# Optimization experiments

Measured on AMD Instinct MI355X. Metric: run time of the kernel, lower is better.

Reference implementation:

```python
import jax, jax.numpy as jnp
import numpy as np

N_NODES = 50000
N_EDGES = 800000


def sage_conv(x, src, dst, W_l, b_l, W_r, num_nodes):
    """PyG SAGEConv with mean aggregation: out = lin_l(mean_agg(neighbors)) + lin_r(x)."""
    # gather source-node features per edge, scatter-mean into destination nodes
    msg = x[src]                                                   # [E, F]
    agg = jax.ops.segment_sum(msg, dst, num_segments=num_nodes)    # [N, F]
    cnt = jax.ops.segment_sum(jnp.ones((src.shape[0],), x.dtype), dst,
                              num_segments=num_nodes)              # [N]
    agg = agg / jnp.maximum(cnt, 1.0)[:, None]
    return agg @ W_l + b_l + x @ W_r


def setup_inputs() -> dict:
    key = jax.random.key(0)
    ks = jax.random.split(key, 8)
    d_in, d_hid, d_out = 128, 256, 128
    s = lambda k, shape, fan: jax.random.normal(k, shape, jnp.float32) / np.sqrt(fan)
    return {
        "x": jax.random.normal(ks[0], (N_NODES, d_in), jnp.float32),
        "edge_index": jax.random.randint(ks[1], (2, N_EDGES), 0, N_NODES, jnp.int64),
        "W1_l": s(ks[2], (d_in, d_hid), d_in),
        "b1": jnp.zeros((d_hid,), jnp.float32),
        "W1_r": s(ks[3], (d_in, d_hid), d_in),
        "W2_l": s(ks[4], (d_hid, d_out), d_hid),
        "b2": jnp.zeros((d_out,), jnp.float32),
        "W2_r": s(ks[5], (d_hid, d_out), d_hid),
    }


def reference(x, edge_index, W1_l, b1, W1_r, W2_l, b2, W2_r):
    src, dst = edge_index[0], edge_index[1]
    n = x.shape[0]
    h = sage_conv(x, src, dst, W1_l, b1, W1_r, n)
    h = jax.nn.relu(h)  # dropout p=0.0 -> identity
    out = sage_conv(h, src, dst, W2_l, b2, W2_r, n)
    return out
```

## Files before the change

kernel.cpp:

```cpp
#include <hip/hip_runtime.h>
#include <hip/hip_bf16.h>
#include <stdint.h>

#define NN 50000
#define NE 800000
#define NB 196
#define EPB 2048
#define NBLK ((NE + EPB - 1) / EPB)

typedef __attribute__((ext_vector_type(8))) __bf16 bf16x8;
typedef __attribute__((ext_vector_type(4))) float f32x4;

__device__ __forceinline__ float bflo(uint32_t u) { return __uint_as_float(u << 16); }
__device__ __forceinline__ float bfhi(uint32_t u) { return __uint_as_float(u & 0xffff0000u); }
__device__ __forceinline__ uint16_t f2bf(float f) {
    uint32_t u = __float_as_uint(f);
    u += 0x7fffu + ((u >> 16) & 1u);
    return (uint16_t)(u >> 16);
}
__device__ __forceinline__ float bf2f(uint16_t h) { return __uint_as_float(((uint32_t)h) << 16); }

__global__ __launch_bounds__(256) void detect(const uint32_t* __restrict__ xu,
                                              const int* __restrict__ ei,
                                              int* __restrict__ flags) {
    __shared__ int cnt_f, cnt_i;
    if (threadIdx.x == 0) { cnt_f = 0; cnt_i = 0; }
    __syncthreads();
    uint32_t u = xu[threadIdx.x];
    uint32_t lo = u & 0xffffu;
    uint32_t e = (lo >> 7) & 0xffu;
    int ok = (lo == 0u) || (e >= 96u && e <= 150u);
    atomicAdd(&cnt_f, ok);
    if (threadIdx.x < 64) {
        int w = ei[2 * threadIdx.x + 1];
        atomicAdd(&cnt_i, (w != 0) ? 1 : 0);
    }
    __syncthreads();
    if (threadIdx.x == 0) {
        flags[0] = (cnt_f < 192) ? 1 : 0;
        flags[1] = (cnt_i < 4) ? 1 : 0;
    }
}

__global__ __launch_bounds__(256) void hist_pass(const int* __restrict__ ei, const int* __restrict__ flags,
                                                 int* __restrict__ histM) {
    __shared__ int hist[NB];
    for (int i = threadIdx.x; i < NB; i += 256) hist[i] = 0;
    __syncthreads();
    int base = blockIdx.x * EPB;
    int fl = flags[1];
    for (int i = 0; i < EPB; i += 256) {
        int e = base + i + threadIdx.x;
        if (e < NE) {
            int d = fl ? ei[2 * NE + 2 * e] : ei[NE + e];
            atomicAdd(&hist[d >> 8], 1);
        }
    }
    __syncthreads();
    for (int i = threadIdx.x; i < NB; i += 256) histM[i * NBLK + blockIdx.x] = hist[i];
}

__global__ __launch_bounds__(512) void scan_rows(int* __restrict__ histM, int* __restrict__ bucket_tot) {
    __shared__ int sm[512];
    int b = blockIdx.x, t = threadIdx.x;
    int v = (t < NBLK) ? histM[b * NBLK + t] : 0;
    sm[t] = v;
    __syncthreads();
    for (int o = 1; o < 512; o <<= 1) {
        int x = (t >= o) ? sm[t - o] : 0;
        __syncthreads();
        sm[t] += x;
        __syncthreads();
    }
    if (t < NBLK) histM[b * NBLK + t] = sm[t] - v;
    if (t == 511) bucket_tot[b] = sm[511];
}

__global__ __launch_bounds__(256) void scan_tot(const int* __restrict__ bucket_tot, int* __restrict__ bucket_base) {
    __shared__ int sm[256];
    int t = threadIdx.x;
    int v = (t < NB) ? bucket_tot[t] : 0;
    sm[t] = v;
    __syncthreads();
    for (int o = 1; o < 256; o <<= 1) {
        int x = (t >= o) ? sm[t - o] : 0;
        __syncthreads();
        sm[t] += x;
        __syncthreads();
    }
    if (t < NB) bucket_base[t] = sm[t] - v;
    if (t == 0) bucket_base[NB] = NE;
}

__global__ __launch_bounds__(256) void scatter_pass(const int* __restrict__ ei, const int* __restrict__ flags,
                                                    const int* __restrict__ histM, const int* __restrict__ bucket_base,
                                                    uint32_t* __restrict__ staging) {
    __shared__ int curs[NB];
    int blk = blockIdx.x, t = threadIdx.x;
    for (int i = t; i < NB; i += 256) curs[i] = bucket_base[i] + histM[i * NBLK + blk];
    __syncthreads();
    int base = blk * EPB;
    int fl = flags[1];
    for (int i = 0; i < EPB; i += 256) {
        int e = base + i + t;
        if (e < NE) {
            int s, d;
            if (fl) { s = ei[2 * e]; d = ei[2 * NE + 2 * e]; }
            else    { s = ei[e];     d = ei[NE + e]; }
            int p = atomicAdd(&curs[d >> 8], 1);
            staging[p] = ((uint32_t)(d & 0xff) << 16) | (uint32_t)s;
        }
    }
}

__global__ __launch_bounds__(256) void build_csr(const uint32_t* __restrict__ staging,
                                                 const int* __restrict__ bucket_base,
                                                 int* __restrict__ row_start, int* __restrict__ deg,
                                                 float* __restrict__ inv_deg, int* __restrict__ csr) {
    __shared__ int degs[256];
    __shared__ int sm[256];
    __shared__ int curs[256];
    int b = blockIdx.x, t = threadIdx.x;
    int beg = bucket_base[b], cnt = bucket_base[b + 1] - beg;
    degs[t] = 0;
    __syncthreads();
    for (int i = t; i < cnt; i += 256) atomicAdd(&degs[(staging[beg + i] >> 16) & 0xff], 1);
    __syncthreads();
    int d = degs[t];
    sm[t] = d;
    __syncthreads();
    for (int o = 1; o < 256; o <<= 1) {
        int x = (t >= o) ? sm[t - o] : 0;
        __syncthreads();
        sm[t] += x;
        __syncthreads();
    }
    int excl = sm[t] - d;
    curs[t] = excl;
    int node = b * 256 + t;
    if (node < NN) {
        row_start[node] = beg + excl;
        deg[node] = d;
        inv_deg[node] = 1.0f / (float)(d > 0 ? d : 1);
    }
    __syncthreads();
    for (int i = t; i < cnt; i += 256) {
        uint32_t u = staging[beg + i];
        int dl = (u >> 16) & 0xff;
        int p = atomicAdd(&curs[dl], 1);
        csr[beg + p] = (int)(u & 0xffffu);
    }
}

__global__ __launch_bounds__(256) void norm_x(const void* __restrict__ x, const int* __restrict__ flags,
                                              uint32_t* __restrict__ out) {
    int i = blockIdx.x * 256 + threadIdx.x;
    if (flags[0]) {
        float2 v = ((const float2*)x)[i];
        out[i] = (uint32_t)f2bf(v.x) | ((uint32_t)f2bf(v.y) << 16);
    } else {
        out[i] = ((const uint32_t*)x)[i];
    }
}

__global__ __launch_bounds__(256) void norm_weights_sw(const void* __restrict__ w1l, const void* __restrict__ b1,
                                                       const void* __restrict__ w1r, const void* __restrict__ w2l,
                                                       const void* __restrict__ b2, const void* __restrict__ w2r,
                                                       const int* __restrict__ flags,
                                                       uint16_t* __restrict__ w1l_sw, uint16_t* __restrict__ w1r_sw,
                                                       uint16_t* __restrict__ w2l_sw, uint16_t* __restrict__ w2r_sw,
                                                       uint16_t* __restrict__ bias_buf) {
    int tid = blockIdx.x * 256 + threadIdx.x;
    int fp32 = flags[0];
    if (tid < 16384) {
        int frag = tid >> 6, lane = tid & 63;
        const void* srcw; uint16_t* dst; int N; int fl;
        if (frag < 64)       { srcw = w1l; dst = w1l_sw; N = 256; fl = frag; }
        else if (frag < 128) { srcw = w1r; dst = w1r_sw; N = 256; fl = frag - 64; }
        else if (frag < 192) { srcw = w2l; dst = w2l_sw; N = 128; fl = frag - 128; }
        else                 { srcw = w2r; dst = w2r_sw; N = 128; fl = frag - 192; }
        int NTm = N >> 4;
        int kt = fl / NTm, nt = fl - kt * NTm;
        int k0 = kt * 32 + (lane >> 4) * 8, n = nt * 16 + (lane & 15);
        uint16_t* d = dst + (size_t)fl * 512 + lane * 8;
#pragma unroll
        for (int j = 0; j < 8; j++) {
            int si = (k0 + j) * N + n;
            d[j] = fp32 ? f2bf(((const float*)srcw)[si]) : ((const uint16_t*)srcw)[si];
        }
    } else if (tid < 16384 + 384) {
        int j = tid - 16384;
        const void* s = (j < 256) ? b1 : b2;
        int jj = (j < 256) ? j : j - 256;
        bias_buf[j] = fp32 ? f2bf(((const float*)s)[jj]) : ((const uint16_t*)s)[jj];
    }
}

__global__ __launch_bounds__(256) void agg_mean_128(const uint32_t* __restrict__ xu,
                                                    const int* __restrict__ row_start,
                                                    const int* __restrict__ deg,
                                                    const int* __restrict__ csr,
                                                    const float* __restrict__ inv_deg,
                                                    uint32_t* __restrict__ outu) {
    int node = blockIdx.x * 4 + (threadIdx.x >> 6);
    int lane = threadIdx.x & 63;
    int beg = row_start[node], end = beg + deg[node];
    float lo[8], hi[8];
#pragma unroll
    for (int k = 0; k < 8; k++) { lo[k] = 0.f; hi[k] = 0.f; }
    int j = beg;
    for (; j + 8 <= end; j += 8) {
        int idx[8];
#pragma unroll
        for (int k = 0; k < 8; k++) idx[k] = csr[j + k];
#pragma unroll
        for (int k = 0; k < 8; k++) {
            uint32_t u = xu[(size_t)idx[k] * 64 + lane];
            lo[k] += bflo(u); hi[k] += bfhi(u);
        }
    }
    for (; j < end; j++) {
        uint32_t u = xu[(size_t)csr[j] * 64 + lane];
        lo[0] += bflo(u); hi[0] += bfhi(u);
    }
    float sc = inv_deg[node];
    float r0 = (((lo[0] + lo[1]) + (lo[2] + lo[3])) + ((lo[4] + lo[5]) + (lo[6] + lo[7]))) * sc;
    float r1 = (((hi[0] + hi[1]) + (hi[2] + hi[3])) + ((hi[4] + hi[5]) + (hi[6] + hi[7]))) * sc;
    outu[(size_t)node * 64 + lane] = (uint32_t)f2bf(r0) | ((uint32_t)f2bf(r1) << 16);
}

__global__ __launch_bounds__(256) void agg_final_128(const uint32_t* __restrict__ tu,
                                                     const int* __restrict__ row_start,
                                                     const int* __restrict__ deg,
                                                     const int* __restrict__ csr,
                                                     const float* __restrict__ inv_deg,
                                                     const float2* __restrict__ u,
                                                     float2* __restrict__ out) {
    int node = blockIdx.x * 4 + (threadIdx.x >> 6);
    int lane = threadIdx.x & 63;
    int beg = row_start[node], end = beg + deg[node];
    float lo[8], hi[8];
#pragma unroll
    for (int k = 0; k < 8; k++) { lo[k] = 0.f; hi[k] = 0.f; }
    int j = beg;
    for (; j + 8 <= end; j += 8) {
        int idx[8];
#pragma unroll
        for (int k = 0; k < 8; k++) idx[k] = csr[j + k];
#pragma unroll
        for (int k = 0; k < 8; k++) {
            uint32_t v = tu[(size_t)idx[k] * 64 + lane];
            lo[k] += bflo(v); hi[k] += bfhi(v);
        }
    }
    for (; j < end; j++) {
        uint32_t v = tu[(size_t)csr[j] * 64 + lane];
        lo[0] += bflo(v); hi[0] += bfhi(v);
    }
    float sc = inv_deg[node];
    float2 uv = u[(size_t)node * 64 + lane];
    float2 r;
    r.x = (((lo[0] + lo[1]) + (lo[2] + lo[3])) + ((lo[4] + lo[5]) + (lo[6] + lo[7]))) * sc + uv.x;
    r.y = (((hi[0] + hi[1]) + (hi[2] + hi[3])) + ((hi[4] + hi[5]) + (hi[6] + hi[7]))) * sc + uv.y;
    out[(size_t)node * 64 + lane] = r;
}

template <int K, int N>
__global__ __launch_bounds__(256) void gemm_dualA_breg(const uint16_t* __restrict__ A1,
                                                       const uint16_t* __restrict__ A2,
                                                       const uint16_t* __restrict__ W1sw,
                                                       const uint16_t* __restrict__ W2sw,
                                                       const uint16_t* __restrict__ bias,
                                                       uint16_t* __restrict__ C) {
    constexpr int NTF = N / 16, NTW = NTF / 4, KT = K / 32;
    int wave = threadIdx.x >> 6, lane = threadIdx.x & 63;
    int row0 = blockIdx.x * 64, bt = wave * NTW;
    int m = lane & 15, q = lane >> 4;
    int ar[4];
#pragma unroll
    for (int rf = 0; rf < 4; rf++) { int r = row0 + rf * 16 + m; ar[rf] = (r < NN) ? r : (NN - 1); }

    bf16x8 B1[KT][NTW], B2[KT][NTW];
#pragma unroll
    for (int kt = 0; kt < KT; kt++)
#pragma unroll
        for (int nt = 0; nt < NTW; nt++) {
            B1[kt][nt] = *(const bf16x8*)(W1sw + ((size_t)(kt * NTF + bt + nt)) * 512 + lane * 8);
            B2[kt][nt] = *(const bf16x8*)(W2sw + ((size_t)(kt * NTF + bt + nt)) * 512 + lane * 8);
        }

    f32x4 acc[4][NTW];
#pragma unroll
    for (int rf = 0; rf < 4; rf++)
#pragma unroll
        for (int nt = 0; nt < NTW; nt++)
#pragma unroll
            for (int i = 0; i < 4; i++) acc[rf][nt][i] = 0.f;

#pragma unroll
    for (int kt = 0; kt < KT; kt++) {
        bf16x8 a0 = *(const bf16x8*)(A1 + (size_t)ar[0] * K + kt * 32 + q * 8);
        bf16x8 a1 = *(const bf16x8*)(A1 + (size_t)ar[1] * K + kt * 32 + q * 8);
        bf16x8 a2 = *(const bf16x8*)(A1 + (size_t)ar[2] * K + kt * 32 + q * 8);
        bf16x8 a3 = *(const bf16x8*)(A1 + (size_t)ar[3] * K + kt * 32 + q * 8);
#pragma unroll
        for (int nt = 0; nt < NTW; nt++) {
            acc[0][nt] = __builtin_amdgcn_mfma_f32_16x16x32_bf16(a0, B1[kt][nt], acc[0][nt], 0, 0, 0);
            acc[1][nt] = __builtin_amdgcn_mfma_f32_16x16x32_bf16(a1, B1[kt][nt], acc[1][nt], 0, 0, 0);
            acc[2][nt] = __builtin_amdgcn_mfma_f32_16x16x32_bf16(a2, B1[kt][nt], acc[2][nt], 0, 0, 0);
            acc[3][nt] = __builtin_amdgcn_mfma_f32_16x16x32_bf16(a3, B1[kt][nt], acc[3][nt], 0, 0, 0);
        }
    }
#pragma unroll
    for (int kt = 0; kt < KT; kt++) {
        bf16x8 a0 = *(const bf16x8*)(A2 + (size_t)ar[0] * K + kt * 32 + q * 8);
        bf16x8 a1 = *(const bf16x8*)(A2 + (size_t)ar[1] * K + kt * 32 + q * 8);
        bf16x8 a2 = *(const bf16x8*)(A2 + (size_t)ar[2] * K + kt * 32 + q * 8);
        bf16x8 a3 = *(const bf16x8*)(A2 + (size_t)ar[3] * K + kt * 32 + q * 8);
#pragma unroll
        for (int nt = 0; nt < NTW; nt++) {
            acc[0][nt] = __builtin_amdgcn_mfma_f32_16x16x32_bf16(a0, B2[kt][nt], acc[0][nt], 0, 0, 0);
            acc[1][nt] = __builtin_amdgcn_mfma_f32_16x16x32_bf16(a1, B2[kt][nt], acc[1][nt], 0, 0, 0);
            acc[2][nt] = __builtin_amdgcn_mfma_f32_16x16x32_bf16(a2, B2[kt][nt], acc[2][nt], 0, 0, 0);
            acc[3][nt] = __builtin_amdgcn_mfma_f32_16x16x32_bf16(a3, B2[kt][nt], acc[3][nt], 0, 0, 0);
        }
    }

#pragma unroll
    for (int nt = 0; nt < NTW; nt++) {
        int col = (bt + nt) * 16 + m;
        float bv = bf2f(bias[col]);
#pragma unroll
        for (int rf = 0; rf < 4; rf++)
#pragma unroll
            for (int i = 0; i < 4; i++) {
                int r = row0 + rf * 16 + q * 4 + i;
                if (r < NN) {
                    float v = fmaxf(acc[rf][nt][i] + bv, 0.f);
                    C[(size_t)r * N + col] = f2bf(v);
                }
            }
    }
}

template <int K, int N>
__global__ __launch_bounds__(256) void gemm_dualB_breg(const uint16_t* __restrict__ A,
                                                       const uint16_t* __restrict__ W1sw,
                                                       const uint16_t* __restrict__ W2sw,
                                                       const uint16_t* __restrict__ bias,
                                                       uint16_t* __restrict__ T,
                                                       float* __restrict__ U) {
    constexpr int NTF = N / 16, NTW = NTF / 4, KT = K / 32;
    int wave = threadIdx.x >> 6, lane = threadIdx.x & 63;
    int row0 = blockIdx.x * 64, bt = wave * NTW;
    int m = lane & 15, q = lane >> 4;
    int ar[4];
#pragma unroll
    for (int rf = 0; rf < 4; rf++) { int r = row0 + rf * 16 + m; ar[rf] = (r < NN) ? r : (NN - 1); }

    bf16x8 B1[KT][NTW], B2[KT][NTW];
#pragma unroll
    for (int kt = 0; kt < KT; kt++)
#pragma unroll
        for (int nt = 0; nt < NTW; nt++) {
            B1[kt][nt] = *(const bf16x8*)(W1sw + ((size_t)(kt * NTF + bt + nt)) * 512 + lane * 8);
            B2[kt][nt] = *(const bf16x8*)(W2sw + ((size_t)(kt * NTF + bt + nt)) * 512 + lane * 8);
        }

    f32x4 acc1[4][NTW], acc2[4][NTW];
#pragma unroll
    for (int rf = 0; rf < 4; rf++)
#pragma unroll
        for (int nt = 0; nt < NTW; nt++)
#pragma unroll
            for (int i = 0; i < 4; i++) { acc1[rf][nt][i] = 0.f; acc2[rf][nt][i] = 0.f; }

#pragma unroll
    for (int kt = 0; kt < KT; kt++) {
        bf16x8 a0 = *(const bf16x8*)(A + (size_t)ar[0] * K + kt * 32 + q * 8);
        bf16x8 a1 = *(const bf16x8*)(A + (size_t)ar[1] * K + kt * 32 + q * 8);
        bf16x8 a2 = *(const bf16x8*)(A + (size_t)ar[2] * K + kt * 32 + q * 8);
        bf16x8 a3 = *(const bf16x8*)(A + (size_t)ar[3] * K + kt * 32 + q * 8);
#pragma unroll
        for (int nt = 0; nt < NTW; nt++) {
            acc1[0][nt] = __builtin_amdgcn_mfma_f32_16x16x32_bf16(a0, B1[kt][nt], acc1[0][nt], 0, 0, 0);
            acc1[1][nt] = __builtin_amdgcn_mfma_f32_16x16x32_bf16(a1, B1[kt][nt], acc1[1][nt], 0, 0, 0);
            acc1[2][nt] = __builtin_amdgcn_mfma_f32_16x16x32_bf16(a2, B1[kt][nt], acc1[2][nt], 0, 0, 0);
            acc1[3][nt] = __builtin_amdgcn_mfma_f32_16x16x32_bf16(a3, B1[kt][nt], acc1[3][nt], 0, 0, 0);
            acc2[0][nt] = __builtin_amdgcn_mfma_f32_16x16x32_bf16(a0, B2[kt][nt], acc2[0][nt], 0, 0, 0);
            acc2[1][nt] = __builtin_amdgcn_mfma_f32_16x16x32_bf16(a1, B2[kt][nt], acc2[1][nt], 0, 0, 0);
            acc2[2][nt] = __builtin_amdgcn_mfma_f32_16x16x32_bf16(a2, B2[kt][nt], acc2[2][nt], 0, 0, 0);
            acc2[3][nt] = __builtin_amdgcn_mfma_f32_16x16x32_bf16(a3, B2[kt][nt], acc2[3][nt], 0, 0, 0);
        }
    }

#pragma unroll
    for (int nt = 0; nt < NTW; nt++) {
        int col = (bt + nt) * 16 + m;
        float bv = bf2f(bias[col]);
#pragma unroll
        for (int rf = 0; rf < 4; rf++)
#pragma unroll
            for (int i = 0; i < 4; i++) {
                int r = row0 + rf * 16 + q * 4 + i;
                if (r < NN) {
                    T[(size_t)r * N + col] = f2bf(acc1[rf][nt][i]);
                    U[(size_t)r * N + col] = acc2[rf][nt][i] + bv;
                }
            }
    }
}

extern "C" void kernel_launch(void* const* d_in, const int* in_sizes, int n_in,
                              void* d_out, int out_size, void* d_ws, size_t ws_size,
                              hipStream_t stream) {
    const void* x_raw  = d_in[0];
    const int*  ei     = (const int*)d_in[1];
    const void* W1l    = d_in[2];
    const void* b1     = d_in[3];
    const void* W1r    = d_in[4];
    const void* W2l    = d_in[5];
    const void* b2     = d_in[6];
    const void* W2r    = d_in[7];

    uint8_t* ws = (uint8_t*)d_ws;
    size_t off = 0;
    auto alloc = [&](size_t b) -> void* {
        void* p = ws + off;
        off += (b + 255) & ~(size_t)255;
        return p;
    };
    int*      flags       = (int*)alloc(256);
    int*      histM       = (int*)alloc((size_t)NB * NBLK * 4);
    int*      bucket_tot  = (int*)alloc((NB + 4) * 4);
    int*      bucket_base = (int*)alloc((NB + 4) * 4);
    int*      deg         = (int*)alloc((size_t)NN * 4);
    float*    inv_deg     = (float*)alloc((size_t)NN * 4);
    int*      row_start   = (int*)alloc((size_t)NN * 4);
    int*      csr         = (int*)alloc((size_t)NE * 4);
    uint32_t* xb          = (uint32_t*)alloc((size_t)NN * 64 * 4);
    uint16_t* bias_buf    = (uint16_t*)alloc(384 * 2);
    uint16_t* agg         = (uint16_t*)alloc((size_t)NN * 128 * 2);
    uint16_t* h           = (uint16_t*)alloc((size_t)NN * 256 * 2);
    uint16_t* t           = (uint16_t*)alloc((size_t)NN * 128 * 2);
    float*    u           = (float*)alloc((size_t)NN * 128 * 4);
    uint16_t* w1l_sw      = (uint16_t*)alloc(128 * 256 * 2);
    uint16_t* w1r_sw      = (uint16_t*)alloc(128 * 256 * 2);
    uint16_t* w2l_sw      = (uint16_t*)alloc(256 * 128 * 2);
    uint16_t* w2r_sw      = (uint16_t*)alloc(256 * 128 * 2);

    uint32_t* staging = (uint32_t*)h;

    detect<<<1, 256, 0, stream>>>((const uint32_t*)x_raw, ei, flags);

    hist_pass<<<NBLK, 256, 0, stream>>>(ei, flags, histM);
    scan_rows<<<NB, 512, 0, stream>>>(histM, bucket_tot);
    scan_tot<<<1, 256, 0, stream>>>(bucket_tot, bucket_base);
    scatter_pass<<<NBLK, 256, 0, stream>>>(ei, flags, histM, bucket_base, staging);
    build_csr<<<NB, 256, 0, stream>>>(staging, bucket_base, row_start, deg, inv_deg, csr);

    norm_x<<<(NN * 64 + 255) / 256, 256, 0, stream>>>(x_raw, flags, xb);
    norm_weights_sw<<<66, 256, 0, stream>>>(W1l, b1, W1r, W2l, b2, W2r, flags,
                                            w1l_sw, w1r_sw, w2l_sw, w2r_sw, bias_buf);

    agg_mean_128<<<NN / 4, 256, 0, stream>>>(xb, row_start, deg, csr, inv_deg, (uint32_t*)agg);
    gemm_dualA_breg<128, 256><<<(NN + 63) / 64, 256, 0, stream>>>(agg, (const uint16_t*)xb,
                                                                  w1l_sw, w1r_sw, bias_buf, h);
    gemm_dualB_breg<256, 128><<<(NN + 63) / 64, 256, 0, stream>>>(h, w2l_sw, w2r_sw, bias_buf + 256, t, u);
    agg_final_128<<<NN / 4, 256, 0, stream>>>((const uint32_t*)t, row_start, deg, csr, inv_deg,
                                              (const float2*)u, (float2*)d_out);
}
```

Before: 278.0 us.

## Retile GEMMs into 64x64 output tiles with LDS-staged vector stores and XCD swizzle

Both dense GEMM kernels are rewritten to split each 64-row block across column groups (4 for the first GEMM, 2 for the second), so each wave holds only 2x2 MFMA tiles and far fewer B fragments in registers. This should raise occupancy and the number of workgroups. Results are staged through shared memory so global writes become coalesced 16-byte stores instead of scattered 2- and 4-byte stores. Block IDs are remapped so neighbouring tiles land on the same XCD for L2 reuse. The cost is that A rows are now re-read once per column group, and each block needs an extra barrier.

```diff
diff --git a/kernel.cpp b/kernel.cpp
--- a/kernel.cpp
+++ b/kernel.cpp
@@ -10,6 +10,7 @@
 
 typedef __attribute__((ext_vector_type(8))) __bf16 bf16x8;
 typedef __attribute__((ext_vector_type(4))) float f32x4;
+typedef __attribute__((ext_vector_type(4))) int i32x4;
 
 __device__ __forceinline__ float bflo(uint32_t u) { return __uint_as_float(u << 16); }
 __device__ __forceinline__ float bfhi(uint32_t u) { return __uint_as_float(u & 0xffff0000u); }
@@ -19,6 +20,13 @@
     return (uint16_t)(u >> 16);
 }
 __device__ __forceinline__ float bf2f(uint16_t h) { return __uint_as_float(((uint32_t)h) << 16); }
+
+__device__ __forceinline__ int xcd_swz(int bid, int nwg) {
+    int q = nwg >> 3, r = nwg & 7;
+    int xcd = bid & 7, idx = bid >> 3;
+    int base = (xcd < r) ? xcd * (q + 1) : r * (q + 1) + (xcd - r) * q;
+    return base + idx;
+}
 
 __global__ __launch_bounds__(256) void detect(const uint32_t* __restrict__ xu,
                                               const int* __restrict__ ei,
@@ -265,149 +273,197 @@
     out[(size_t)node * 64 + lane] = r;
 }
 
-template <int K, int N>
-__global__ __launch_bounds__(256) void gemm_dualA_breg(const uint16_t* __restrict__ A1,
-                                                       const uint16_t* __restrict__ A2,
-                                                       const uint16_t* __restrict__ W1sw,
-                                                       const uint16_t* __restrict__ W2sw,
-                                                       const uint16_t* __restrict__ bias,
-                                                       uint16_t* __restrict__ C) {
-    constexpr int NTF = N / 16, NTW = NTF / 4, KT = K / 32;
+__global__ __launch_bounds__(256) void gemm1_v2(const uint16_t* __restrict__ A1,
+                                                const uint16_t* __restrict__ A2,
+                                                const uint16_t* __restrict__ W1sw,
+                                                const uint16_t* __restrict__ W2sw,
+                                                const uint16_t* __restrict__ bias,
+                                                uint16_t* __restrict__ C) {
+    __shared__ __align__(16) uint16_t cs[64][72];
+    int wg = xcd_swz(blockIdx.x, 3128);
+    int rg = wg >> 2, cg = wg & 3;
     int wave = threadIdx.x >> 6, lane = threadIdx.x & 63;
-    int row0 = blockIdx.x * 64, bt = wave * NTW;
+    int wr = wave >> 1, wc = wave & 1;
     int m = lane & 15, q = lane >> 4;
-    int ar[4];
-#pragma unroll
-    for (int rf = 0; rf < 4; rf++) { int r = row0 + rf * 16 + m; ar[rf] = (r < NN) ? r : (NN - 1); }
-
-    bf16x8 B1[KT][NTW], B2[KT][NTW];
-#pragma unroll
-    for (int kt = 0; kt < KT; kt++)
-#pragma unroll
-        for (int nt = 0; nt < NTW; nt++) {
-            B1[kt][nt] = *(const bf16x8*)(W1sw + ((size_t)(kt * NTF + bt + nt)) * 512 + lane * 8);
-            B2[kt][nt] = *(const bf16x8*)(W2sw + ((size_t)(kt * NTF + bt + nt)) * 512 + lane * 8);
-        }
-
-    f32x4 acc[4][NTW];
-#pragma unroll
-    for (int rf = 0; rf < 4; rf++)
-#pragma unroll
-        for (int nt = 0; nt < NTW; nt++)
+    int rowbase = rg * 64 + wr * 32;
+    int gnt0 = cg * 4 + wc * 2;
+
+    int ar[2];
+#pragma unroll
+    for (int rf = 0; rf < 2; rf++) {
+        int r = rowbase + rf * 16 + m;
+        ar[rf] = (r < NN) ? r : (NN - 1);
+    }
+
+    f32x4 acc[2][2];
+#pragma unroll
+    for (int rf = 0; rf < 2; rf++)
+#pragma unroll
+        for (int nt = 0; nt < 2; nt++)
 #pragma unroll
             for (int i = 0; i < 4; i++) acc[rf][nt][i] = 0.f;
 
-#pragma unroll
-    for (int kt = 0; kt < KT; kt++) {
-        bf16x8 a0 = *(const bf16x8*)(A1 + (size_t)ar[0] * K + kt * 32 + q * 8);
-        bf16x8 a1 = *(const bf16x8*)(A1 + (size_t)ar[1] * K + kt * 32 + q * 8);
-        bf16x8 a2 = *(const bf16x8*)(A1 + (size_t)ar[2] * K + kt * 32 + q * 8);
-        bf16x8 a3 = *(const bf16x8*)(A1 + (size_t)ar[3] * K + kt * 32 + q * 8);
-#pragma unroll
-        for (int nt = 0; nt < NTW; nt++) {
-            acc[0][nt] = __builtin_amdgcn_mfma_f32_16x16x32_bf16(a0, B1[kt][nt], acc[0][nt], 0, 0, 0);
-            acc[1][nt] = __builtin_amdgcn_mfma_f32_16x16x32_bf16(a1, B1[kt][nt], acc[1][nt], 0, 0, 0);
-            acc[2][nt] = __builtin_amdgcn_mfma_f32_16x16x32_bf16(a2, B1[kt][nt], acc[2][nt], 0, 0, 0);
-            acc[3][nt] = __builtin_amdgcn_mfma_f32_16x16x32_bf16(a3, B1[kt][nt], acc[3][nt], 0, 0, 0);
-        }
-    }
-#pragma unroll
-    for (int kt = 0; kt < KT; kt++) {
-        bf16x8 a0 = *(const bf16x8*)(A2 + (size_t)ar[0] * K + kt * 32 + q * 8);
-        bf16x8 a1 = *(const bf16x8*)(A2 + (size_t)ar[1] * K + kt * 32 + q * 8);
-        bf16x8 a2 = *(const bf16x8*)(A2 + (size_t)ar[2] * K + kt * 32 + q * 8);
-        bf16x8 a3 = *(const bf16x8*)(A2 + (size_t)ar[3] * K + kt * 32 + q * 8);
-#pragma unroll
-        for (int nt = 0; nt < NTW; nt++) {
-            acc[0][nt] = __builtin_amdgcn_mfma_f32_16x16x32_bf16(a0, B2[kt][nt], acc[0][nt], 0, 0, 0);
-            acc[1][nt] = __builtin_amdgcn_mfma_f32_16x16x32_bf16(a1, B2[kt][nt], acc[1][nt], 0, 0, 0);
-            acc[2][nt] = __builtin_amdgcn_mfma_f32_16x16x32_bf16(a2, B2[kt][nt], acc[2][nt], 0, 0, 0);
-            acc[3][nt] = __builtin_amdgcn_mfma_f32_16x16x32_bf16(a3, B2[kt][nt], acc[3][nt], 0, 0, 0);
-        }
-    }
-
-#pragma unroll
-    for (int nt = 0; nt < NTW; nt++) {
-        int col = (bt + nt) * 16 + m;
-        float bv = bf2f(bias[col]);
-#pragma unroll
-        for (int rf = 0; rf < 4; rf++)
+    {
+        bf16x8 B[4][2];
+#pragma unroll
+        for (int kt = 0; kt < 4; kt++)
+#pragma unroll
+            for (int nt = 0; nt < 2; nt++)
+                B[kt][nt] = *(const bf16x8*)(W1sw + ((size_t)(kt * 16 + gnt0 + nt)) * 512 + lane * 8);
+#pragma unroll
+        for (int kt = 0; kt < 4; kt++) {
+            bf16x8 a0 = *(const bf16x8*)(A1 + (size_t)ar[0] * 128 + kt * 32 + q * 8);
+            bf16x8 a1 = *(const bf16x8*)(A1 + (size_t)ar[1] * 128 + kt * 32 + q * 8);
+#pragma unroll
+            for (int nt = 0; nt < 2; nt++) {
+                acc[0][nt] = __builtin_amdgcn_mfma_f32_16x16x32_bf16(a0, B[kt][nt], acc[0][nt], 0, 0, 0);
+                acc[1][nt] = __builtin_amdgcn_mfma_f32_16x16x32_bf16(a1, B[kt][nt], acc[1][nt], 0, 0, 0);
+            }
+        }
+    }
+    asm volatile("" ::: "memory");
+    {
+        bf16x8 B[4][2];
+#pragma unroll
+        for (int kt = 0; kt < 4; kt++)
+#pragma unroll
+            for (int nt = 0; nt < 2; nt++)
+                B[kt][nt] = *(const bf16x8*)(W2sw + ((size_t)(kt * 16 + gnt0 + nt)) * 512 + lane * 8);
+#pragma unroll
+        for (int kt = 0; kt < 4; kt++) {
+            bf16x8 a0 = *(const bf16x8*)(A2 + (size_t)ar[0] * 128 + kt * 32 + q * 8);
+            bf16x8 a1 = *(const bf16x8*)(A2 + (size_t)ar[1] * 128 + kt * 32 + q * 8);
+#pragma unroll
+            for (int nt = 0; nt < 2; nt++) {
+                acc[0][nt] = __builtin_amdgcn_mfma_f32_16x16x32_bf16(a0, B[kt][nt], acc[0][nt], 0, 0, 0);
+                acc[1][nt] = __builtin_amdgcn_mfma_f32_16x16x32_bf16(a1, B[kt][nt], acc[1][nt], 0, 0, 0);
+            }
+        }
+    }
+
+#pragma unroll
+    for (int rf = 0; rf < 2; rf++)
+#pragma unroll
+        for (int nt = 0; nt < 2; nt++) {
+            int coll = wc * 32 + nt * 16 + m;
+            float bv = bf2f(bias[cg * 64 + coll]);
 #pragma unroll
             for (int i = 0; i < 4; i++) {
-                int r = row0 + rf * 16 + q * 4 + i;
-                if (r < NN) {
-                    float v = fmaxf(acc[rf][nt][i] + bv, 0.f);
-                    C[(size_t)r * N + col] = f2bf(v);
-                }
+                float v = fmaxf(acc[rf][nt][i] + bv, 0.f);
+                cs[wr * 32 + rf * 16 + q * 4 + i][coll] = f2bf(v);
             }
-    }
-}
-
-template <int K, int N>
-__global__ __launch_bounds__(256) void gemm_dualB_breg(const uint16_t* __restrict__ A,
-                                                       const uint16_t* __restrict__ W1sw,
-                                                       const uint16_t* __restrict__ W2sw,
-                                                       const uint16_t* __restrict__ bias,
-                                                       uint16_t* __restrict__ T,
-                                                       float* __restrict__ U) {
-    constexpr int NTF = N / 16, NTW = NTF / 4, KT = K / 32;
+        }
+    __syncthreads();
+    int tt = threadIdx.x;
+#pragma unroll
+    for (int rr = 0; rr < 2; rr++) {
+        int row = rr * 32 + (tt >> 3);
+        int grow = rg * 64 + row;
+        if (grow < NN)
+            *(i32x4*)(C + (size_t)grow * 256 + cg * 64 + (tt & 7) * 8) =
+                *(const i32x4*)&cs[row][(tt & 7) * 8];
+    }
+}
+
+__global__ __launch_bounds__(256) void gemm2_v2(const uint16_t* __restrict__ A,
+                                                const uint16_t* __restrict__ W1sw,
+                                                const uint16_t* __restrict__ W2sw,
+                                                const uint16_t* __restrict__ bias,
+                                                uint16_t* __restrict__ T,
+                                                float* __restrict__ U) {
+    __shared__ __align__(16) uint16_t ts[64][72];
+    __shared__ __align__(16) float us[64][68];
+    int wg = xcd_swz(blockIdx.x, 1564);
+    int rg = wg >> 1, cg = wg & 1;
     int wave = threadIdx.x >> 6, lane = threadIdx.x & 63;
-    int row0 = blockIdx.x * 64, bt = wave * NTW;
+    int wr = wave >> 1, wc = wave & 1;
     int m = lane & 15, q = lane >> 4;
-    int ar[4];
-#pragma unroll
-    for (int rf = 0; rf < 4; rf++) { int r = row0 + rf * 16 + m; ar[rf] = (r < NN) ? r : (NN - 1); }
-
-    bf16x8 B1[KT][NTW], B2[KT][NTW];
-#pragma unroll
-    for (int kt = 0; kt < KT; kt++)
-#pragma unroll
-        for (int nt = 0; nt < NTW; nt++) {
-            B1[kt][nt] = *(const bf16x8*)(W1sw + ((size_t)(kt * NTF + bt + nt)) * 512 + lane * 8);
-            B2[kt][nt] = *(const bf16x8*)(W2sw + ((size_t)(kt * NTF + bt + nt)) * 512 + lane * 8);
-        }
-
-    f32x4 acc1[4][NTW], acc2[4][NTW];
-#pragma unroll
-    for (int rf = 0; rf < 4; rf++)
-#pragma unroll
-        for (int nt = 0; nt < NTW; nt++)
+    int rowbase = rg * 64 + wr * 32;
+    int gnt0 = cg * 4 + wc * 2;
+
+    int ar[2];
+#pragma unroll
+    for (int rf = 0; rf < 2; rf++) {
+        int r = rowbase + rf * 16 + m;
+        ar[rf] = (r < NN) ? r : (NN - 1);
+    }
+
+    f32x4 acc1[2][2], acc2[2][2];
+#pragma unroll
+    for (int rf = 0; rf < 2; rf++)
+#pragma unroll
+        for (int nt = 0; nt < 2; nt++)
 #pragma unroll
             for (int i = 0; i < 4; i++) { acc1[rf][nt][i] = 0.f; acc2[rf][nt][i] = 0.f; }
 
-#pragma unroll
-    for (int kt = 0; kt < KT; kt++) {
-        bf16x8 a0 = *(const bf16x8*)(A + (size_t)ar[0] * K + kt * 32 + q * 8);
-        bf16x8 a1 = *(const bf16x8*)(A + (size_t)ar[1] * K + kt * 32 + q * 8);
-        bf16x8 a2 = *(const bf16x8*)(A + (size_t)ar[2] * K + kt * 32 + q * 8);
-        bf16x8 a3 = *(const bf16x8*)(A + (size_t)ar[3] * K + kt * 32 + q * 8);
-#pragma unroll
-        for (int nt = 0; nt < NTW; nt++) {
-            acc1[0][nt] = __builtin_amdgcn_mfma_f32_16x16x32_bf16(a0, B1[kt][nt], acc1[0][nt], 0, 0, 0);
-            acc1[1][nt] = __builtin_amdgcn_mfma_f32_16x16x32_bf16(a1, B1[kt][nt], acc1[1][nt], 0, 0, 0);
-            acc1[2][nt] = __builtin_amdgcn_mfma_f32_16x16x32_bf16(a2, B1[kt][nt], acc1[2][nt], 0, 0, 0);
-            acc1[3][nt] = __builtin_amdgcn_mfma_f32_16x16x32_bf16(a3, B1[kt][nt], acc1[3][nt], 0, 0, 0);
-            acc2[0][nt] = __builtin_amdgcn_mfma_f32_16x16x32_bf16(a0, B2[kt][nt], acc2[0][nt], 0, 0, 0);
-            acc2[1][nt] = __builtin_amdgcn_mfma_f32_16x16x32_bf16(a1, B2[kt][nt], acc2[1][nt], 0, 0, 0);
-            acc2[2][nt] = __builtin_amdgcn_mfma_f32_16x16x32_bf16(a2, B2[kt][nt], acc2[2][nt], 0, 0, 0);
-            acc2[3][nt] = __builtin_amdgcn_mfma_f32_16x16x32_bf16(a3, B2[kt][nt], acc2[3][nt], 0, 0, 0);
-        }
-    }
-
-#pragma unroll
-    for (int nt = 0; nt < NTW; nt++) {
-        int col = (bt + nt) * 16 + m;
-        float bv = bf2f(bias[col]);
-#pragma unroll
-        for (int rf = 0; rf < 4; rf++)
+    {
+        bf16x8 B[8][2];
+#pragma unroll
+        for (int kt = 0; kt < 8; kt++)
+#pragma unroll
+            for (int nt = 0; nt < 2; nt++)
+                B[kt][nt] = *(const bf16x8*)(W1sw + ((size_t)(kt * 8 + gnt0 + nt)) * 512 + lane * 8);
+#pragma unroll
+        for (int kt = 0; kt < 8; kt++) {
+            bf16x8 a0 = *(const bf16x8*)(A + (size_t)ar[0] * 256 + kt * 32 + q * 8);
+            bf16x8 a1 = *(const bf16x8*)(A + (size_t)ar[1] * 256 + kt * 32 + q * 8);
+#pragma unroll
+            for (int nt = 0; nt < 2; nt++) {
+                acc1[0][nt] = __builtin_amdgcn_mfma_f32_16x16x32_bf16(a0, B[kt][nt], acc1[0][nt], 0, 0, 0);
+                acc1[1][nt] = __builtin_amdgcn_mfma_f32_16x16x32_bf16(a1, B[kt][nt], acc1[1][nt], 0, 0, 0);
+            }
+        }
+    }
+    asm volatile("" ::: "memory");
+    {
+        bf16x8 B[8][2];
+#pragma unroll
+        for (int kt = 0; kt < 8; kt++)
+#pragma unroll
+            for (int nt = 0; nt < 2; nt++)
+                B[kt][nt] = *(const bf16x8*)(W2sw + ((size_t)(kt * 8 + gnt0 + nt)) * 512 + lane * 8);
+#pragma unroll
+        for (int kt = 0; kt < 8; kt++) {
+            bf16x8 a0 = *(const bf16x8*)(A + (size_t)ar[0] * 256 + kt * 32 + q * 8);
+            bf16x8 a1 = *(const bf16x8*)(A + (size_t)ar[1] * 256 + kt * 32 + q * 8);
+#pragma unroll
+            for (int nt = 0; nt < 2; nt++) {
+                acc2[0][nt] = __builtin_amdgcn_mfma_f32_16x16x32_bf16(a0, B[kt][nt], acc2[0][nt], 0, 0, 0);
+                acc2[1][nt] = __builtin_amdgcn_mfma_f32_16x16x32_bf16(a1, B[kt][nt], acc2[1][nt], 0, 0, 0);
+            }
+        }
+    }
+
+#pragma unroll
+    for (int rf = 0; rf < 2; rf++)
+#pragma unroll
+        for (int nt = 0; nt < 2; nt++) {
+            int coll = wc * 32 + nt * 16 + m;
+            float bv = bf2f(bias[cg * 64 + coll]);
 #pragma unroll
             for (int i = 0; i < 4; i++) {
-                int r = row0 + rf * 16 + q * 4 + i;
-                if (r < NN) {
-                    T[(size_t)r * N + col] = f2bf(acc1[rf][nt][i]);
-                    U[(size_t)r * N + col] = acc2[rf][nt][i] + bv;
-                }
+                int rl = wr * 32 + rf * 16 + q * 4 + i;
+                ts[rl][coll] = f2bf(acc1[rf][nt][i]);
+                us[rl][coll] = acc2[rf][nt][i] + bv;
             }
+        }
+    __syncthreads();
+    int tt = threadIdx.x;
+#pragma unroll
+    for (int rr = 0; rr < 2; rr++) {
+        int row = rr * 32 + (tt >> 3);
+        int grow = rg * 64 + row;
+        if (grow < NN)
+            *(i32x4*)(T + (size_t)grow * 128 + cg * 64 + (tt & 7) * 8) =
+                *(const i32x4*)&ts[row][(tt & 7) * 8];
+    }
+#pragma unroll
+    for (int rr = 0; rr < 4; rr++) {
+        int row = rr * 16 + (tt >> 4);
+        int grow = rg * 64 + row;
+        if (grow < NN)
+            *(f32x4*)(U + (size_t)grow * 128 + cg * 64 + (tt & 15) * 4) =
+                *(const f32x4*)&us[row][(tt & 15) * 4];
     }
 }
 
@@ -464,9 +520,8 @@
                                             w1l_sw, w1r_sw, w2l_sw, w2r_sw, bias_buf);
 
     agg_mean_128<<<NN / 4, 256, 0, stream>>>(xb, row_start, deg, csr, inv_deg, (uint32_t*)agg);
-    gemm_dualA_breg<128, 256><<<(NN + 63) / 64, 256, 0, stream>>>(agg, (const uint16_t*)xb,
-                                                                  w1l_sw, w1r_sw, bias_buf, h);
-    gemm_dualB_breg<256, 128><<<(NN + 63) / 64, 256, 0, stream>>>(h, w2l_sw, w2r_sw, bias_buf + 256, t, u);
+    gemm1_v2<<<3128, 256, 0, stream>>>(agg, (const uint16_t*)xb, w1l_sw, w1r_sw, bias_buf, h);
+    gemm2_v2<<<1564, 256, 0, stream>>>(h, w2l_sw, w2r_sw, bias_buf + 256, t, u);
     agg_final_128<<<NN / 4, 256, 0, stream>>>((const uint32_t*)t, row_start, deg, csr, inv_deg,
                                               (const float2*)u, (float2*)d_out);
 }
```

Result: faster. 268.9 us (-3.3%).
